# Kernel tuning notes

Hardware: AMD Instinct MI355X
Metric: run time of the kernel (lower is better)

## Reference

```python
import jax, jax.numpy as jnp
import numpy as np

NUM_HEADS = 8
KEY_DIM = 256
EPS = 1e-16


def setup_inputs() -> dict:
    key = jax.random.key(0)
    k1, k2, k3, k4 = jax.random.split(key, 4)
    b, n, d, m = 2, 20000, 256, 320000
    q = jax.random.normal(k1, (b, n, d), dtype=jnp.float32)
    k = jax.random.normal(k2, (b, n, d), dtype=jnp.float32)
    e = jax.random.randint(k3, (2, m), 0, n, dtype=jnp.int64)
    r = jax.random.randint(k4, (m,), 0, n, dtype=jnp.int64)
    return {"q": q, "k": k, "e": e, "r": r}


def reference(q, k, e, r):
    b, n, d = q.shape
    m = e.shape[1]
    dh = d // NUM_HEADS
    # gather edge endpoints, multiply, sum within each head's d_head chunk
    # (scatter_sum over dim with h=[i//dh] == reshape + sum over last axis)
    src_q = q[:, e[0], :]                      # (b, m, d)
    dst_k = k[:, e[1], :]                      # (b, m, d)
    a = (src_q * dst_k).reshape(b, m, NUM_HEADS, dh).sum(-1)  # (b, m, H)
    a = a / jnp.sqrt(jnp.asarray(KEY_DIM, a.dtype))
    # segment softmax over edges grouped by r (global max subtraction, as in source)
    a = a - a.max()
    ex = jnp.exp(a)                            # (b, m, H)
    seg = jax.ops.segment_sum(ex.transpose(1, 0, 2), r, num_segments=n)  # (n, b, H)
    denom = seg[r].transpose(1, 0, 2)          # (b, m, H)
    return ex / (denom + EPS)
```

## Files before the change

kernel.cpp:

```cpp
#include <hip/hip_runtime.h>
#include <hip/hip_bf16.h>
#include <cmath>

#define D 256
#define NH 8
#define B 2
#define EPW 4
#define NBKMAX 1024
#define NCHMAX 512
#define SBLK 1024
#define NSUP 8

#if defined(__has_builtin)
#  if __has_builtin(__builtin_amdgcn_fdot2_f32_bf16)
#    define USE_BF16_DOT 1
#  else
#    define USE_BF16_DOT 0
#  endif
#else
#  define USE_BF16_DOT 0
#endif

#if USE_BF16_DOT
typedef __bf16 bf16x2 __attribute__((ext_vector_type(2)));
#endif

__device__ inline unsigned short f2bf(float f) {
    unsigned u = __float_as_uint(f);
    unsigned r = u + 0x7FFFu + ((u >> 16) & 1u);
    return (unsigned short)(r >> 16);
}

__device__ inline float dot16(const uint4& a, const uint4& b) {
    float p = 0.f;
#if USE_BF16_DOT
    const bf16x2* av = (const bf16x2*)&a;
    const bf16x2* bv = (const bf16x2*)&b;
    #pragma unroll
    for (int w = 0; w < 4; ++w)
        p = __builtin_amdgcn_fdot2_f32_bf16(av[w], bv[w], p, false);
#else
    const unsigned* aw = (const unsigned*)&a;
    const unsigned* bw = (const unsigned*)&b;
    #pragma unroll
    for (int w = 0; w < 4; ++w) {
        float al = __uint_as_float(aw[w] << 16);
        float ah = __uint_as_float(aw[w] & 0xFFFF0000u);
        float bl = __uint_as_float(bw[w] << 16);
        float bh = __uint_as_float(bw[w] & 0xFFFF0000u);
        p = fmaf(al, bl, p);
        p = fmaf(ah, bh, p);
    }
#endif
    return p;
}

__device__ inline int edge_key(int e0, int e1, int sdiv, int nb1) {
    return (e0 / sdiv) * nb1 + (e1 >> 8);
}

__global__ __launch_bounds__(256) void k_conv(
    const float* __restrict__ q, const float* __restrict__ k,
    uint4* __restrict__ qc, uint4* __restrict__ kc,
    float* __restrict__ seg, int segN, int n)
{
    int tid    = blockIdx.x * blockDim.x + threadIdx.x;
    int stride = gridDim.x * blockDim.x;
    for (int i = tid; i < segN; i += stride) seg[i] = 0.f;
    int total = n * B * 32;
    for (int i = tid; i < total; i += stride) {
        int c   = i & 31;
        int row = i >> 5;
        int bb  = (row >= n) ? 1 : 0;
        int node = row - bb * n;
        const float4* qs = (const float4*)(q + ((size_t)row << 8)) + (c << 1);
        const float4* ks = (const float4*)(k + ((size_t)row << 8)) + (c << 1);
        float4 a0 = qs[0], a1 = qs[1];
        float4 b0 = ks[0], b1 = ks[1];
        uint4 pa, pb;
        pa.x = (unsigned)f2bf(a0.x) | ((unsigned)f2bf(a0.y) << 16);
        pa.y = (unsigned)f2bf(a0.z) | ((unsigned)f2bf(a0.w) << 16);
        pa.z = (unsigned)f2bf(a1.x) | ((unsigned)f2bf(a1.y) << 16);
        pa.w = (unsigned)f2bf(a1.z) | ((unsigned)f2bf(a1.w) << 16);
        pb.x = (unsigned)f2bf(b0.x) | ((unsigned)f2bf(b0.y) << 16);
        pb.y = (unsigned)f2bf(b0.z) | ((unsigned)f2bf(b0.w) << 16);
        pb.z = (unsigned)f2bf(b1.x) | ((unsigned)f2bf(b1.y) << 16);
        pb.w = (unsigned)f2bf(b1.z) | ((unsigned)f2bf(b1.w) << 16);
        size_t dst = ((size_t)node * B + bb) * 32 + c;
        qc[dst] = pa;
        kc[dst] = pb;
    }
}


__global__ __launch_bounds__(256) void k_hist2(
    const int* __restrict__ e, int* __restrict__ bh, int m, int nbk,
    int sdiv, int nb1)
{
    __shared__ int lh[NBKMAX];
    int b = blockIdx.x;
    int start = b * SBLK, end = min(m, start + SBLK);
    for (int t = threadIdx.x; t < nbk; t += 256) lh[t] = 0;
    __syncthreads();
    for (int j = start + threadIdx.x; j < end; j += 256)
        atomicAdd(&lh[edge_key(e[j], e[m + j], sdiv, nb1)], 1);
    __syncthreads();
    for (int t = threadIdx.x; t < nbk; t += 256)
        bh[(size_t)b * nbk + t] = lh[t];
}

__global__ __launch_bounds__(NCHMAX) void k_colscan(
    int* __restrict__ bh, int* __restrict__ tot, int nch, int nbk)
{
    __shared__ int tmp[NCHMAX];
    int t = blockIdx.x;
    int b = threadIdx.x;
    int v = (b < nch) ? bh[(size_t)b * nbk + t] : 0;
    tmp[b] = v;
    __syncthreads();
    for (int off = 1; off < NCHMAX; off <<= 1) {
        int u = (b >= off) ? tmp[b - off] : 0;
        __syncthreads();
        tmp[b] += u;
        __syncthreads();
    }
    if (b < nch) bh[(size_t)b * nbk + t] = tmp[b] - v;
    if (b == NCHMAX - 1) tot[t] = tmp[b];
}

__global__ __launch_bounds__(NBKMAX) void k_basescan(
    const int* __restrict__ tot, int* __restrict__ base, int nbk)
{
    __shared__ int tmp[NBKMAX];
    int t = threadIdx.x;
    int v = (t < nbk) ? tot[t] : 0;
    tmp[t] = v;
    __syncthreads();
    for (int off = 1; off < NBKMAX; off <<= 1) {
        int u = (t >= off) ? tmp[t - off] : 0;
        __syncthreads();
        tmp[t] += u;
        __syncthreads();
    }
    if (t < nbk) base[t] = tmp[t] - v;
}

__global__ __launch_bounds__(256) void k_scatter2(
    const int* __restrict__ e, const int* __restrict__ r,
    const int* __restrict__ bh, const int* __restrict__ base,
    int4* __restrict__ perm, int m, int nbk, int sdiv, int nb1)
{
    __shared__ int cur[NBKMAX];
    int b = blockIdx.x;
    int start = b * SBLK, end = min(m, start + SBLK);
    for (int t = threadIdx.x; t < nbk; t += 256)
        cur[t] = bh[(size_t)b * nbk + t] + base[t];
    __syncthreads();
    for (int j = start + threadIdx.x; j < end; j += 256) {
        int e0 = e[j], e1 = e[m + j];
        int pos = atomicAdd(&cur[edge_key(e0, e1, sdiv, nb1)], 1);
        perm[pos] = make_int4(e0, e1, r[j], j);
    }
}

__global__ __launch_bounds__(256) void k_scores_perm(
    const ushort* __restrict__ qc, const ushort* __restrict__ kc,
    const int4* __restrict__ perm,
    float* __restrict__ s, float* __restrict__ seg, int m, int do_swz)
{
    int bid = blockIdx.x;
    if (do_swz) {
        int nb8 = gridDim.x >> 3;
        bid = (bid & 7) * nb8 + (bid >> 3);
    }
    int wave = (bid << 2) + (threadIdx.x >> 6);
    int lane = threadIdx.x & 63;
    int j0 = wave * EPW;
    if (j0 >= m) return;

    int rr[EPW], jo[EPW];
    uint4 qa[EPW], kb[EPW];
    #pragma unroll
    for (int t = 0; t < EPW; ++t) {
        int j = j0 + t;
        int4 p = (j < m) ? perm[j] : make_int4(0, 0, 0, -1);
        rr[t] = p.z;
        jo[t] = p.w;
        qa[t] = ((const uint4*)(qc + (size_t)p.x * (B * D)))[lane];
        kb[t] = ((const uint4*)(kc + (size_t)p.y * (B * D)))[lane];
    }
    __builtin_amdgcn_sched_barrier(0);

    #pragma unroll
    for (int t = 0; t < EPW; ++t) {
        float p = dot16(qa[t], kb[t]);
        p += __shfl_xor(p, 1);
        p += __shfl_xor(p, 2);
        float ex = __expf(p * 0.0625f);
        if ((lane & 3) == 0 && jo[t] >= 0) {
            int bb = lane >> 5;
            int h  = (lane >> 2) & 7;
            s[((size_t)bb * m + jo[t]) * NH + h] = ex;
            atomicAdd(&seg[((size_t)rr[t] * B + bb) * NH + h], ex);
        }
    }
}

__global__ __launch_bounds__(256) void k_scores_fused(
    const ushort* __restrict__ qc, const ushort* __restrict__ kc,
    const int* __restrict__ e, const int* __restrict__ r,
    float* __restrict__ s, float* __restrict__ seg, int m)
{
    int wave = (int)((blockIdx.x * blockDim.x + threadIdx.x) >> 6);
    int lane = threadIdx.x & 63;
    int j0 = wave * EPW;
    if (j0 >= m) return;

    int e0[EPW], e1[EPW], rr[EPW];
    #pragma unroll
    for (int t = 0; t < EPW; ++t) {
        int j = j0 + t;
        int ok = (j < m);
        e0[t] = ok ? e[j]     : 0;
        e1[t] = ok ? e[m + j] : 0;
        rr[t] = ok ? r[j]     : 0;
    }
    uint4 qa[EPW], kb[EPW];
    #pragma unroll
    for (int t = 0; t < EPW; ++t) {
        qa[t] = ((const uint4*)(qc + (size_t)e0[t] * (B * D)))[lane];
        kb[t] = ((const uint4*)(kc + (size_t)e1[t] * (B * D)))[lane];
    }
    __builtin_amdgcn_sched_barrier(0);
    #pragma unroll
    for (int t = 0; t < EPW; ++t) {
        float p = dot16(qa[t], kb[t]);
        p += __shfl_xor(p, 1);
        p += __shfl_xor(p, 2);
        float ex = __expf(p * 0.0625f);
        if ((lane & 3) == 0 && (j0 + t) < m) {
            int bb = lane >> 5;
            int h  = (lane >> 2) & 7;
            s[((size_t)bb * m + (j0 + t)) * NH + h] = ex;
            atomicAdd(&seg[((size_t)rr[t] * B + bb) * NH + h], ex);
        }
    }
}

__global__ __launch_bounds__(256) void k_scores_fused_f32(
    const float* __restrict__ q, const float* __restrict__ k,
    const int* __restrict__ e, const int* __restrict__ r,
    float* __restrict__ s, float* __restrict__ seg, int n, int m)
{
    int wave = (int)((blockIdx.x * blockDim.x + threadIdx.x) >> 6);
    int lane = threadIdx.x & 63;
    int j0 = wave * EPW;
    if (j0 >= m) return;
    int e0[EPW], e1[EPW], rr[EPW];
    #pragma unroll
    for (int t = 0; t < EPW; ++t) {
        int j = j0 + t; int ok = (j < m);
        e0[t] = ok ? e[j] : 0; e1[t] = ok ? e[m + j] : 0; rr[t] = ok ? r[j] : 0;
    }
    float4 qa[B][EPW], kb[B][EPW];
    #pragma unroll
    for (int bb = 0; bb < B; ++bb)
        #pragma unroll
        for (int t = 0; t < EPW; ++t) {
            qa[bb][t] = ((const float4*)(q + ((size_t)bb * n + e0[t]) * D))[lane];
            kb[bb][t] = ((const float4*)(k + ((size_t)bb * n + e1[t]) * D))[lane];
        }
    #pragma unroll
    for (int bb = 0; bb < B; ++bb)
        #pragma unroll
        for (int t = 0; t < EPW; ++t) {
            float4 A = qa[bb][t], K4 = kb[bb][t];
            float p = A.x * K4.x + A.y * K4.y + A.z * K4.z + A.w * K4.w;
            p += __shfl_xor(p, 1); p += __shfl_xor(p, 2); p += __shfl_xor(p, 4);
            float ex = __expf(p * 0.0625f);
            if ((lane & 7) == 0 && (j0 + t) < m) {
                int h = lane >> 3;
                s[((size_t)bb * m + (j0 + t)) * NH + h] = ex;
                atomicAdd(&seg[((size_t)rr[t] * B + bb) * NH + h], ex);
            }
        }
}

__global__ __launch_bounds__(256) void k_norm(
    float* __restrict__ s, const int* __restrict__ r,
    const float* __restrict__ seg, int m)
{
    int i = blockIdx.x * blockDim.x + threadIdx.x;
    int total = B * m;
    if (i >= total) return;
    int bb = (i >= m) ? 1 : 0;
    int j  = i - bb * m;
    const float4* sg = (const float4*)(seg + ((size_t)r[j] * B + bb) * NH);
    float4* sp = (float4*)(s + (size_t)i * NH);
    float4 d0 = sg[0], d1 = sg[1];
    float4 x0 = sp[0], x1 = sp[1];
    x0.x = __fdividef(x0.x, d0.x + 1e-16f);
    x0.y = __fdividef(x0.y, d0.y + 1e-16f);
    x0.z = __fdividef(x0.z, d0.z + 1e-16f);
    x0.w = __fdividef(x0.w, d0.w + 1e-16f);
    x1.x = __fdividef(x1.x, d1.x + 1e-16f);
    x1.y = __fdividef(x1.y, d1.y + 1e-16f);
    x1.z = __fdividef(x1.z, d1.z + 1e-16f);
    x1.w = __fdividef(x1.w, d1.w + 1e-16f);
    sp[0] = x0; sp[1] = x1;
}

extern "C" void kernel_launch(void* const* d_in, const int* in_sizes, int n_in,
                              void* d_out, int out_size, void* d_ws, size_t ws_size,
                              hipStream_t stream) {
    const float* q = (const float*)d_in[0];
    const float* k = (const float*)d_in[1];
    const int*   e = (const int*)d_in[2];
    const int*   r = (const int*)d_in[3];
    float* s = (float*)d_out;

    int n = in_sizes[0] / (B * D);
    int m = in_sizes[3];
    int sdiv = (n + NSUP - 1) / NSUP;
    int nb1  = (n + 255) >> 8;
    int nbk  = NSUP * nb1;
    int nch  = (m + SBLK - 1) / SBLK;
    int segN = n * B * NH;

    size_t seg_bytes  = (size_t)segN * sizeof(float);
    size_t row_bytes  = (size_t)n * B * D * sizeof(unsigned short);
    size_t perm_bytes = (size_t)m * sizeof(int4);
    size_t bh_bytes   = (size_t)nch * nbk * sizeof(int);
    size_t tb_bytes   = 2 * NBKMAX * sizeof(int);

    float*  seg  = (float*)d_ws;
    ushort* qc   = (ushort*)((char*)d_ws + seg_bytes);
    ushort* kc   = (ushort*)((char*)d_ws + seg_bytes + row_bytes);
    int4*   perm = (int4*)((char*)d_ws + seg_bytes + 2 * row_bytes);
    int*    bh   = (int*)((char*)d_ws + seg_bytes + 2 * row_bytes + perm_bytes);
    int*    tot  = (int*)((char*)bh + bh_bytes);
    int*    base = tot + NBKMAX;

    bool use_bf16 = ws_size >= (seg_bytes + 2 * row_bytes);
    bool use_sort = use_bf16 && nbk <= NBKMAX && nch <= NCHMAX &&
                    ws_size >= (seg_bytes + 2 * row_bytes + perm_bytes +
                                bh_bytes + tb_bytes);

    int nblocks = (B * m + 255) / 256;
    int nwaves  = (m + EPW - 1) / EPW;
    int sblocks = (nwaves + 3) / 4;

    if (use_bf16) {
        int cblocks = (n * B * 32 + 255) / 256;
        k_conv<<<cblocks, 256, 0, stream>>>(q, k, (uint4*)qc, (uint4*)kc,
                                            seg, segN, n);
        if (use_sort) {
            k_hist2<<<nch, 256, 0, stream>>>(e, bh, m, nbk, sdiv, nb1);
            k_colscan<<<nbk, NCHMAX, 0, stream>>>(bh, tot, nch, nbk);
            k_basescan<<<1, NBKMAX, 0, stream>>>(tot, base, nbk);
            k_scatter2<<<nch, 256, 0, stream>>>(e, r, bh, base, perm, m, nbk,
                                                sdiv, nb1);
            int do_swz = (sblocks % 8 == 0) ? 1 : 0;
            k_scores_perm<<<sblocks, 256, 0, stream>>>(qc, kc, perm, s, seg, m, do_swz);
        } else {
            k_scores_fused<<<sblocks, 256, 0, stream>>>(qc, kc, e, r, s, seg, m);
        }
    } else {
        hipMemsetAsync(d_ws, 0, seg_bytes, stream);
        k_scores_fused_f32<<<sblocks, 256, 0, stream>>>(q, k, e, r, s, seg, n, m);
    }
    k_norm<<<nblocks, 256, 0, stream>>>(s, r, seg, m);
}
```

Baseline: 209.5 us.

## Sort edges by source node with fine buckets and in-bucket radix subsort

The 2D bucketing (source super-bucket × destination chunk of 256) becomes 1D bucketing by source node in groups of 64. A new shared-memory counting-sort kernel then orders each bucket by the low 6 bits of the source index, so edges come out fully sorted by source. The goal is that consecutive waves reuse the same q rows. The cost is the loss of destination-side locality, which makes k gathers random, plus one extra kernel launch.

```diff
diff --git a/kernel.cpp b/kernel.cpp
--- a/kernel.cpp
+++ b/kernel.cpp
@@ -9,7 +9,7 @@
 #define NBKMAX 1024
 #define NCHMAX 512
 #define SBLK 1024
-#define NSUP 8
+#define SUBCAP 2048
 
 #if defined(__has_builtin)
 #  if __has_builtin(__builtin_amdgcn_fdot2_f32_bf16)
@@ -56,7 +56,8 @@
 }
 
 __device__ inline int edge_key(int e0, int e1, int sdiv, int nb1) {
-    return (e0 / sdiv) * nb1 + (e1 >> 8);
+    int kminor = (nb1 > 1) ? (e1 >> 8) : 0;
+    return (e0 / sdiv) * nb1 + kminor;
 }
 
 __global__ __launch_bounds__(256) void k_conv(
@@ -163,6 +164,34 @@
     }
 }
 
+__global__ __launch_bounds__(256) void k_subsort(
+    int4* __restrict__ perm, const int* __restrict__ base, int m, int nbk)
+{
+    __shared__ int4 buf[SUBCAP];
+    __shared__ int hist[64], off[64];
+    int t = blockIdx.x;
+    int start = base[t];
+    int end   = (t + 1 < nbk) ? base[t + 1] : m;
+    int len   = end - start;
+    if (len <= 1 || len > SUBCAP) return;
+    for (int i = threadIdx.x; i < len; i += 256) buf[i] = perm[start + i];
+    if (threadIdx.x < 64) hist[threadIdx.x] = 0;
+    __syncthreads();
+    for (int i = threadIdx.x; i < len; i += 256)
+        atomicAdd(&hist[buf[i].x & 63], 1);
+    __syncthreads();
+    if (threadIdx.x == 0) {
+        int run = 0;
+        #pragma unroll
+        for (int i = 0; i < 64; ++i) { off[i] = run; run += hist[i]; }
+    }
+    __syncthreads();
+    for (int i = threadIdx.x; i < len; i += 256) {
+        int pos = atomicAdd(&off[buf[i].x & 63], 1);
+        perm[start + pos] = buf[i];
+    }
+}
+
 __global__ __launch_bounds__(256) void k_scores_perm(
     const ushort* __restrict__ qc, const ushort* __restrict__ kc,
     const int4* __restrict__ perm,
@@ -321,9 +350,9 @@
 
     int n = in_sizes[0] / (B * D);
     int m = in_sizes[3];
-    int sdiv = (n + NSUP - 1) / NSUP;
-    int nb1  = (n + 255) >> 8;
-    int nbk  = NSUP * nb1;
+    int sdiv = 64;
+    int nb1  = 1;
+    int nbk  = (n + 63) >> 6;
     int nch  = (m + SBLK - 1) / SBLK;
     int segN = n * B * NH;
 
@@ -360,6 +389,7 @@
             k_basescan<<<1, NBKMAX, 0, stream>>>(tot, base, nbk);
             k_scatter2<<<nch, 256, 0, stream>>>(e, r, bh, base, perm, m, nbk,
                                                 sdiv, nb1);
+            k_subsort<<<nbk, 256, 0, stream>>>(perm, base, m, nbk);
             int do_swz = (sblocks % 8 == 0) ? 1 : 0;
             k_scores_perm<<<sblocks, 256, 0, stream>>>(qc, kc, perm, s, seg, m, do_swz);
         } else {
```

Result: no change. 211.7 us (+1.1%).

## Bucket edges by source node only and fold base scan into scatter

Applied to the files above, without the earlier changes.

Replaces the 2D edge bucketing key (source super-block by destination block of 256 nodes) with a 1D key on source node shifted by 5, giving about 625 buckets. The separate single-block base-scan kernel is removed; each scatter block recomputes the prefix over bucket totals in shared memory. This drops one launch and the integer divide in the key, but the edge ordering now groups only by source, so destination k-row gathers lose locality and L2 reuse in the scores kernel may change.

```diff
diff --git a/kernel.cpp b/kernel.cpp
--- a/kernel.cpp
+++ b/kernel.cpp
@@ -6,10 +6,10 @@
 #define NH 8
 #define B 2
 #define EPW 4
+#define SSH 5
 #define NBKMAX 1024
 #define NCHMAX 512
 #define SBLK 1024
-#define NSUP 8
 
 #if defined(__has_builtin)
 #  if __has_builtin(__builtin_amdgcn_fdot2_f32_bf16)
@@ -53,10 +53,6 @@
     }
 #endif
     return p;
-}
-
-__device__ inline int edge_key(int e0, int e1, int sdiv, int nb1) {
-    return (e0 / sdiv) * nb1 + (e1 >> 8);
 }
 
 __global__ __launch_bounds__(256) void k_conv(
@@ -94,8 +90,7 @@
 
 
 __global__ __launch_bounds__(256) void k_hist2(
-    const int* __restrict__ e, int* __restrict__ bh, int m, int nbk,
-    int sdiv, int nb1)
+    const int* __restrict__ e, int* __restrict__ bh, int m, int nbk)
 {
     __shared__ int lh[NBKMAX];
     int b = blockIdx.x;
@@ -103,7 +98,7 @@
     for (int t = threadIdx.x; t < nbk; t += 256) lh[t] = 0;
     __syncthreads();
     for (int j = start + threadIdx.x; j < end; j += 256)
-        atomicAdd(&lh[edge_key(e[j], e[m + j], sdiv, nb1)], 1);
+        atomicAdd(&lh[e[j] >> SSH], 1);
     __syncthreads();
     for (int t = threadIdx.x; t < nbk; t += 256)
         bh[(size_t)b * nbk + t] = lh[t];
@@ -128,37 +123,45 @@
     if (b == NCHMAX - 1) tot[t] = tmp[b];
 }
 
-__global__ __launch_bounds__(NBKMAX) void k_basescan(
-    const int* __restrict__ tot, int* __restrict__ base, int nbk)
-{
-    __shared__ int tmp[NBKMAX];
-    int t = threadIdx.x;
-    int v = (t < nbk) ? tot[t] : 0;
-    tmp[t] = v;
-    __syncthreads();
-    for (int off = 1; off < NBKMAX; off <<= 1) {
-        int u = (t >= off) ? tmp[t - off] : 0;
-        __syncthreads();
-        tmp[t] += u;
-        __syncthreads();
-    }
-    if (t < nbk) base[t] = tmp[t] - v;
-}
-
 __global__ __launch_bounds__(256) void k_scatter2(
     const int* __restrict__ e, const int* __restrict__ r,
-    const int* __restrict__ bh, const int* __restrict__ base,
-    int4* __restrict__ perm, int m, int nbk, int sdiv, int nb1)
-{
+    const int* __restrict__ bh, const int* __restrict__ tot,
+    int4* __restrict__ perm, int m, int nbk)
+{
+    __shared__ int tl[NBKMAX];
+    __shared__ int tp[256];
+    int b = blockIdx.x;
+    int tid = threadIdx.x;
+    for (int i = tid; i < NBKMAX; i += 256)
+        tl[i] = (i < nbk) ? tot[i] : 0;
+    __syncthreads();
+    int s0 = tl[tid * 4 + 0], s1 = tl[tid * 4 + 1];
+    int s2 = tl[tid * 4 + 2], s3 = tl[tid * 4 + 3];
+    tl[tid * 4 + 0] = 0;
+    tl[tid * 4 + 1] = s0;
+    tl[tid * 4 + 2] = s0 + s1;
+    tl[tid * 4 + 3] = s0 + s1 + s2;
+    int v = s0 + s1 + s2 + s3;
+    tp[tid] = v;
+    __syncthreads();
+    for (int off = 1; off < 256; off <<= 1) {
+        int u = (tid >= off) ? tp[tid - off] : 0;
+        __syncthreads();
+        tp[tid] += u;
+        __syncthreads();
+    }
+    int stripbase = tp[tid] - v;
+    #pragma unroll
+    for (int j2 = 0; j2 < 4; ++j2) tl[tid * 4 + j2] += stripbase;
+    __syncthreads();
     __shared__ int cur[NBKMAX];
-    int b = blockIdx.x;
+    for (int t = tid; t < nbk; t += 256)
+        cur[t] = bh[(size_t)b * nbk + t] + tl[t];
+    __syncthreads();
     int start = b * SBLK, end = min(m, start + SBLK);
-    for (int t = threadIdx.x; t < nbk; t += 256)
-        cur[t] = bh[(size_t)b * nbk + t] + base[t];
-    __syncthreads();
-    for (int j = start + threadIdx.x; j < end; j += 256) {
+    for (int j = start + tid; j < end; j += 256) {
         int e0 = e[j], e1 = e[m + j];
-        int pos = atomicAdd(&cur[edge_key(e0, e1, sdiv, nb1)], 1);
+        int pos = atomicAdd(&cur[e0 >> SSH], 1);
         perm[pos] = make_int4(e0, e1, r[j], j);
     }
 }
@@ -321,9 +324,7 @@
 
     int n = in_sizes[0] / (B * D);
     int m = in_sizes[3];
-    int sdiv = (n + NSUP - 1) / NSUP;
-    int nb1  = (n + 255) >> 8;
-    int nbk  = NSUP * nb1;
+    int nbk  = (n + (1 << SSH) - 1) >> SSH;
     int nch  = (m + SBLK - 1) / SBLK;
     int segN = n * B * NH;
 
@@ -331,7 +332,7 @@
     size_t row_bytes  = (size_t)n * B * D * sizeof(unsigned short);
     size_t perm_bytes = (size_t)m * sizeof(int4);
     size_t bh_bytes   = (size_t)nch * nbk * sizeof(int);
-    size_t tb_bytes   = 2 * NBKMAX * sizeof(int);
+    size_t tb_bytes   = NBKMAX * sizeof(int);
 
     float*  seg  = (float*)d_ws;
     ushort* qc   = (ushort*)((char*)d_ws + seg_bytes);
@@ -339,7 +340,6 @@
     int4*   perm = (int4*)((char*)d_ws + seg_bytes + 2 * row_bytes);
     int*    bh   = (int*)((char*)d_ws + seg_bytes + 2 * row_bytes + perm_bytes);
     int*    tot  = (int*)((char*)bh + bh_bytes);
-    int*    base = tot + NBKMAX;
 
     bool use_bf16 = ws_size >= (seg_bytes + 2 * row_bytes);
     bool use_sort = use_bf16 && nbk <= NBKMAX && nch <= NCHMAX &&
@@ -355,11 +355,9 @@
         k_conv<<<cblocks, 256, 0, stream>>>(q, k, (uint4*)qc, (uint4*)kc,
                                             seg, segN, n);
         if (use_sort) {
-            k_hist2<<<nch, 256, 0, stream>>>(e, bh, m, nbk, sdiv, nb1);
+            k_hist2<<<nch, 256, 0, stream>>>(e, bh, m, nbk);
             k_colscan<<<nbk, NCHMAX, 0, stream>>>(bh, tot, nch, nbk);
-            k_basescan<<<1, NBKMAX, 0, stream>>>(tot, base, nbk);
-            k_scatter2<<<nch, 256, 0, stream>>>(e, r, bh, base, perm, m, nbk,
-                                                sdiv, nb1);
+            k_scatter2<<<nch, 256, 0, stream>>>(e, r, bh, tot, perm, m, nbk);
             int do_swz = (sblocks % 8 == 0) ? 1 : 0;
             k_scores_perm<<<sblocks, 256, 0, stream>>>(qc, kc, perm, s, seg, m, do_swz);
         } else {
```

New measurement: 207.1 us, median of 2. No clear change (-1.1%).
